# Performance work log

Hardware: AMD Instinct MI355X
Metric: run time of the kernel (lower is better)

## Reference

```python
import jax, jax.numpy as jnp
import numpy as np
from jax import lax

WIN_SIZE = 11
BANDWIDTH = 0.5


def _regression(rand, target, win_size, bandwidth):
    """Sliding-window bandwidth-weighted regression moments.

    For each pixel p, over window neighbors q:
      w_pq = exp(-||target_p - target_q||^2 / bandwidth^2)   (guide-based kernel)
      x  = sum_q w * t_q / wgtSum
      xx = sum_q w * t_q^2 / wgtSum
      xy = sum_q w * t_q * r_q / wgtSum
      y  = sum_q w * r_q / wgtSum
    """
    B, H, W, C = target.shape
    R = win_size // 2
    inv_bw2 = 1.0 / (bandwidth * bandwidth)

    pad_cfg = ((0, 0), (R, R), (R, R), (0, 0))
    t_pad = jnp.pad(target, pad_cfg)
    r_pad = jnp.pad(rand, pad_cfg)
    # validity mask so out-of-image taps contribute zero weight
    m_pad = jnp.pad(jnp.ones((B, H, W, 1), dtype=target.dtype), pad_cfg)

    # all (dy, dx) offsets in the window, scanned sequentially (static count)
    offs = np.stack(np.meshgrid(np.arange(win_size), np.arange(win_size),
                                indexing='ij'), axis=-1).reshape(-1, 2)
    offs = jnp.asarray(offs, dtype=jnp.int32)

    zeros_c = jnp.zeros((B, H, W, C), dtype=target.dtype)
    zeros_1 = jnp.zeros((B, H, W, 1), dtype=target.dtype)

    def body(carry, off):
        x, xx, xy, y, wsum = carry
        dy, dx = off[0], off[1]
        t_s = lax.dynamic_slice(t_pad, (0, dy, dx, 0), (B, H, W, C))
        r_s = lax.dynamic_slice(r_pad, (0, dy, dx, 0), (B, H, W, C))
        m_s = lax.dynamic_slice(m_pad, (0, dy, dx, 0), (B, H, W, 1))
        # per-pixel squared color distance on the guide, summed over channels
        d = jnp.sum((target - t_s) ** 2, axis=-1, keepdims=True)  # [B,H,W,1]
        w = jnp.exp(-d * inv_bw2) * m_s                           # [B,H,W,1]
        return (x + w * t_s,
                xx + w * t_s * t_s,
                xy + w * t_s * r_s,
                y + w * r_s,
                wsum + w), None

    (x, xx, xy, y, wsum), _ = lax.scan(
        body, (zeros_c, zeros_c, zeros_c, zeros_c, zeros_1), offs)

    inv_w = 1.0 / wsum  # wsum >= 1 (center tap has w=1), safe
    return x * inv_w, xx * inv_w, xy * inv_w, y * inv_w


def setup_inputs() -> dict:
    key = jax.random.key(0)
    k1, k2 = jax.random.split(key)
    B, H, W, C = 4, 720, 1280, 3
    rand = jax.random.uniform(k1, (B, H, W, C), dtype=jnp.float32)
    target = jax.random.uniform(k2, (B, H, W, C), dtype=jnp.float32)
    return {"rand": rand, "target": target}


def reference(rand, target):
    return _regression(rand, target, WIN_SIZE, BANDWIDTH)
```

## Files before the change

### kernel.cpp

```cpp
#include <hip/hip_runtime.h>


#define HH   720
#define WW   1280
#define BB   4
#define RAD  5
#define TX   64
#define TY   16
#define KX   4
#define LW   74
#define LH   26
#define LSTR 75
#define PLANE (LSTR * LH)
#define LDS_FLOATS 12288

__global__ __launch_bounds__(256, 3)
void regression_kernel(const float* __restrict__ rnd,
                       const float* __restrict__ tgt,
                       float* __restrict__ out)
{
    __shared__ __align__(16) float lds[LDS_FLOATS];
    float* pt0 = lds;
    float* pt1 = lds + PLANE;
    float* pt2 = lds + 2 * PLANE;
    float* pr0 = lds + 3 * PLANE;
    float* pr1 = lds + 4 * PLANE;
    float* pr2 = lds + 5 * PLANE;

    const int tx = threadIdx.x;
    const int ty = threadIdx.y;
    const int tid = ty * 16 + tx;
    const int X0 = blockIdx.x * TX;
    const int Y0 = blockIdx.y * TY;
    const int b  = blockIdx.z;

    for (int i = tid; i < LW * LH; i += 256) {
        int ly = i / LW;
        int lx = i - ly * LW;
        int gy = Y0 + ly - RAD;
        int gx = X0 + lx - RAD;
        float t0 = 0.f, t1 = 0.f, t2 = 0.f, r0 = 0.f, r1 = 0.f, r2 = 0.f;
        if ((unsigned)gy < (unsigned)HH && (unsigned)gx < (unsigned)WW) {
            int off = ((b * HH + gy) * WW + gx) * 3;
            t0 = tgt[off + 0]; t1 = tgt[off + 1]; t2 = tgt[off + 2];
            r0 = rnd[off + 0]; r1 = rnd[off + 1]; r2 = rnd[off + 2];
        }
        int s = ly * LSTR + lx;
        pt0[s] = t0; pt1[s] = t1; pt2[s] = t2;
        pr0[s] = r0; pr1[s] = r1; pr2[s] = r2;
    }
    __syncthreads();

    float tp0[KX], tp1[KX], tp2[KX];
    {
        int s = (ty + RAD) * LSTR + tx * KX + RAD;
        #pragma unroll
        for (int k = 0; k < KX; ++k) {
            tp0[k] = pt0[s + k]; tp1[k] = pt1[s + k]; tp2[k] = pt2[s + k];
        }
    }

    float sx0[KX] = {}, sx1[KX] = {}, sx2[KX] = {};
    float sxx0[KX] = {}, sxx1[KX] = {}, sxx2[KX] = {};
    float sxy0[KX] = {}, sxy1[KX] = {}, sxy2[KX] = {};
    float sy0[KX] = {}, sy1[KX] = {}, sy2[KX] = {};
    float sw[KX] = {};

    const int xbase = X0 + tx * KX - RAD;
    const int ybase = Y0 + ty - RAD;
    const float NEG = -1e30f;
    const float CC  = -5.770780163555852f;

    #pragma unroll 1
    for (int dy = 0; dy < 11; ++dy) {
        const float rowbias = ((unsigned)(ybase + dy) < (unsigned)HH) ? 0.f : NEG;
        const int rbase = (ty + dy) * LSTR + tx * KX;
        #pragma unroll
        for (int j = 0; j < 14; ++j) {
            const int s = rbase + j;
            const float t0 = pt0[s], t1 = pt1[s], t2 = pt2[s];
            const float r0 = pr0[s], r1 = pr1[s], r2 = pr2[s];
            const float bias = ((unsigned)(xbase + j) < (unsigned)WW) ? rowbias : NEG;
            #pragma unroll
            for (int k = 0; k < KX; ++k) {
                if (j >= k && j <= k + 10) {
                    float d0 = tp0[k] - t0;
                    float d1 = tp1[k] - t1;
                    float d2 = tp2[k] - t2;
                    float d  = d0 * d0;
                    d = fmaf(d1, d1, d);
                    d = fmaf(d2, d2, d);
                    float w = exp2f(fmaf(d, CC, bias));
                    float wt0 = w * t0, wt1 = w * t1, wt2 = w * t2;
                    sx0[k] += wt0;  sx1[k] += wt1;  sx2[k] += wt2;
                    sxx0[k] = fmaf(wt0, t0, sxx0[k]);
                    sxx1[k] = fmaf(wt1, t1, sxx1[k]);
                    sxx2[k] = fmaf(wt2, t2, sxx2[k]);
                    sxy0[k] = fmaf(wt0, r0, sxy0[k]);
                    sxy1[k] = fmaf(wt1, r1, sxy1[k]);
                    sxy2[k] = fmaf(wt2, r2, sxy2[k]);
                    sy0[k]  = fmaf(w, r0, sy0[k]);
                    sy1[k]  = fmaf(w, r1, sy1[k]);
                    sy2[k]  = fmaf(w, r2, sy2[k]);
                    sw[k]  += w;
                }
            }
        }
    }

    float inv[KX];
    #pragma unroll
    for (int k = 0; k < KX; ++k) inv[k] = 1.0f / sw[k];

    __syncthreads();

    float4* l4 = (float4*)lds;
    {
        const int b4 = ty * 48 + tx * 3;
#define STAGE_CHUNK(a0, a1, a2, cidx)                                          \
        {                                                                      \
            float4* p = l4 + (cidx) * 768 + b4;                                \
            p[0] = make_float4(a0[0]*inv[0], a1[0]*inv[0], a2[0]*inv[0],       \
                               a0[1]*inv[1]);                                  \
            p[1] = make_float4(a1[1]*inv[1], a2[1]*inv[1], a0[2]*inv[2],       \
                               a1[2]*inv[2]);                                  \
            p[2] = make_float4(a2[2]*inv[2], a0[3]*inv[3], a1[3]*inv[3],       \
                               a2[3]*inv[3]);                                  \
        }
        STAGE_CHUNK(sx0,  sx1,  sx2,  0)
        STAGE_CHUNK(sxx0, sxx1, sxx2, 1)
        STAGE_CHUNK(sxy0, sxy1, sxy2, 2)
        STAGE_CHUNK(sy0,  sy1,  sy2,  3)
#undef STAGE_CHUNK
    }
    __syncthreads();

    const int CH = BB * HH * WW * 3;
    int rr[3], cc4[3];
    #pragma unroll
    for (int m = 0; m < 3; ++m) {
        int r = m * 256 + tid;
        rr[m]  = r / 48;
        cc4[m] = r - rr[m] * 48;
    }
    #pragma unroll
    for (int i = 0; i < 12; ++i) {
        const int c = i / 3;
        const int m = i - c * 3;
        float4 v = l4[c * 768 + m * 256 + tid];
        const int gaddr = c * CH + ((b * HH + Y0 + rr[m]) * WW + X0) * 3 + cc4[m] * 4;
        *(float4*)(out + gaddr) = v;
    }
}

extern "C" void kernel_launch(void* const* d_in, const int* in_sizes, int n_in,
                              void* d_out, int out_size, void* d_ws, size_t ws_size,
                              hipStream_t stream) {
    const float* rnd = (const float*)d_in[0];
    const float* tgt = (const float*)d_in[1];
    float* out = (float*)d_out;

    dim3 grid(WW / TX, HH / TY, BB);
    dim3 block(16, 16);
    regression_kernel<<<grid, block, 0, stream>>>(rnd, tgt, out);
}
```

Before: 684.3 us.

## Use sentinel guide values for padding and vectorize LDS row loads

Out-of-image taps are now filled with a huge sentinel guide value, so their Gaussian weight underflows to zero. This removes the per-tap row/column bias computation and the extra FMA in the exponent. The LDS stride is padded to 76 so each thread's row window can be read with aligned float4 loads in two chunks of 8 and 6 taps, replacing scalar LDS reads. This relies on exp2 of a very large negative argument returning exactly zero, and the 16-wide reads per thread may raise LDS bank pressure.

```diff
diff --git a/kernel.cpp b/kernel.cpp
--- a/kernel.cpp
+++ b/kernel.cpp
@@ -8,9 +8,8 @@
 #define TX   64
 #define TY   16
 #define KX   4
-#define LW   74
 #define LH   26
-#define LSTR 75
+#define LSTR 76
 #define PLANE (LSTR * LH)
 #define LDS_FLOATS 12288
 
@@ -34,20 +33,21 @@
     const int Y0 = blockIdx.y * TY;
     const int b  = blockIdx.z;
 
-    for (int i = tid; i < LW * LH; i += 256) {
-        int ly = i / LW;
-        int lx = i - ly * LW;
+    const float SENT = 1e19f;
+
+    for (int i = tid; i < PLANE; i += 256) {
+        int ly = i / LSTR;
+        int lx = i - ly * LSTR;
         int gy = Y0 + ly - RAD;
         int gx = X0 + lx - RAD;
-        float t0 = 0.f, t1 = 0.f, t2 = 0.f, r0 = 0.f, r1 = 0.f, r2 = 0.f;
+        float t0 = SENT, t1 = SENT, t2 = SENT, r0 = 0.f, r1 = 0.f, r2 = 0.f;
         if ((unsigned)gy < (unsigned)HH && (unsigned)gx < (unsigned)WW) {
             int off = ((b * HH + gy) * WW + gx) * 3;
             t0 = tgt[off + 0]; t1 = tgt[off + 1]; t2 = tgt[off + 2];
             r0 = rnd[off + 0]; r1 = rnd[off + 1]; r2 = rnd[off + 2];
         }
-        int s = ly * LSTR + lx;
-        pt0[s] = t0; pt1[s] = t1; pt2[s] = t2;
-        pr0[s] = r0; pr1[s] = r1; pr2[s] = r2;
+        pt0[i] = t0; pt1[i] = t1; pt2[i] = t2;
+        pr0[i] = r0; pr1[i] = r1; pr2[i] = r2;
     }
     __syncthreads();
 
@@ -66,47 +66,83 @@
     float sy0[KX] = {}, sy1[KX] = {}, sy2[KX] = {};
     float sw[KX] = {};
 
-    const int xbase = X0 + tx * KX - RAD;
-    const int ybase = Y0 + ty - RAD;
-    const float NEG = -1e30f;
-    const float CC  = -5.770780163555852f;
+    const float CC = -5.770780163555852f;
+
+#define TAPK(k)                                                         \
+    {                                                                   \
+        float d0 = tp0[k] - t0;                                         \
+        float d1 = tp1[k] - t1;                                         \
+        float d2 = tp2[k] - t2;                                         \
+        float d  = d0 * d0;                                             \
+        d = fmaf(d1, d1, d);                                            \
+        d = fmaf(d2, d2, d);                                            \
+        float w = exp2f(d * CC);         \
+        float wt0 = w * t0, wt1 = w * t1, wt2 = w * t2;                 \
+        sx0[k] += wt0;  sx1[k] += wt1;  sx2[k] += wt2;                  \
+        sxx0[k] = fmaf(wt0, t0, sxx0[k]);                               \
+        sxx1[k] = fmaf(wt1, t1, sxx1[k]);                               \
+        sxx2[k] = fmaf(wt2, t2, sxx2[k]);                               \
+        sxy0[k] = fmaf(wt0, r0, sxy0[k]);                               \
+        sxy1[k] = fmaf(wt1, r1, sxy1[k]);                               \
+        sxy2[k] = fmaf(wt2, r2, sxy2[k]);                               \
+        sy0[k]  = fmaf(w, r0, sy0[k]);                                  \
+        sy1[k]  = fmaf(w, r1, sy1[k]);                                  \
+        sy2[k]  = fmaf(w, r2, sy2[k]);                                  \
+        sw[k]  += w;                                                    \
+    }
 
     #pragma unroll 1
     for (int dy = 0; dy < 11; ++dy) {
-        const float rowbias = ((unsigned)(ybase + dy) < (unsigned)HH) ? 0.f : NEG;
-        const int rbase = (ty + dy) * LSTR + tx * KX;
+        const int rb = (ty + dy) * LSTR + tx * KX;
+        float T0[8], T1[8], T2[8], R0[8], R1[8], R2[8];
+
+        *(float4*)&T0[0] = *(const float4*)(pt0 + rb);
+        *(float4*)&T0[4] = *(const float4*)(pt0 + rb + 4);
+        *(float4*)&T1[0] = *(const float4*)(pt1 + rb);
+        *(float4*)&T1[4] = *(const float4*)(pt1 + rb + 4);
+        *(float4*)&T2[0] = *(const float4*)(pt2 + rb);
+        *(float4*)&T2[4] = *(const float4*)(pt2 + rb + 4);
+        *(float4*)&R0[0] = *(const float4*)(pr0 + rb);
+        *(float4*)&R0[4] = *(const float4*)(pr0 + rb + 4);
+        *(float4*)&R1[0] = *(const float4*)(pr1 + rb);
+        *(float4*)&R1[4] = *(const float4*)(pr1 + rb + 4);
+        *(float4*)&R2[0] = *(const float4*)(pr2 + rb);
+        *(float4*)&R2[4] = *(const float4*)(pr2 + rb + 4);
+
         #pragma unroll
-        for (int j = 0; j < 14; ++j) {
-            const int s = rbase + j;
-            const float t0 = pt0[s], t1 = pt1[s], t2 = pt2[s];
-            const float r0 = pr0[s], r1 = pr1[s], r2 = pr2[s];
-            const float bias = ((unsigned)(xbase + j) < (unsigned)WW) ? rowbias : NEG;
+        for (int j = 0; j < 8; ++j) {
+            const float t0 = T0[j], t1 = T1[j], t2 = T2[j];
+            const float r0 = R0[j], r1 = R1[j], r2 = R2[j];
             #pragma unroll
-            for (int k = 0; k < KX; ++k) {
-                if (j >= k && j <= k + 10) {
-                    float d0 = tp0[k] - t0;
-                    float d1 = tp1[k] - t1;
-                    float d2 = tp2[k] - t2;
-                    float d  = d0 * d0;
-                    d = fmaf(d1, d1, d);
-                    d = fmaf(d2, d2, d);
-                    float w = exp2f(fmaf(d, CC, bias));
-                    float wt0 = w * t0, wt1 = w * t1, wt2 = w * t2;
-                    sx0[k] += wt0;  sx1[k] += wt1;  sx2[k] += wt2;
-                    sxx0[k] = fmaf(wt0, t0, sxx0[k]);
-                    sxx1[k] = fmaf(wt1, t1, sxx1[k]);
-                    sxx2[k] = fmaf(wt2, t2, sxx2[k]);
-                    sxy0[k] = fmaf(wt0, r0, sxy0[k]);
-                    sxy1[k] = fmaf(wt1, r1, sxy1[k]);
-                    sxy2[k] = fmaf(wt2, r2, sxy2[k]);
-                    sy0[k]  = fmaf(w, r0, sy0[k]);
-                    sy1[k]  = fmaf(w, r1, sy1[k]);
-                    sy2[k]  = fmaf(w, r2, sy2[k]);
-                    sw[k]  += w;
-                }
-            }
-        }
-    }
+            for (int k = 0; k < KX; ++k)
+                if (k <= j)
+                    TAPK(k)
+        }
+
+        *(float4*)&T0[0] = *(const float4*)(pt0 + rb + 8);
+        *(float4*)&T0[4] = *(const float4*)(pt0 + rb + 12);
+        *(float4*)&T1[0] = *(const float4*)(pt1 + rb + 8);
+        *(float4*)&T1[4] = *(const float4*)(pt1 + rb + 12);
+        *(float4*)&T2[0] = *(const float4*)(pt2 + rb + 8);
+        *(float4*)&T2[4] = *(const float4*)(pt2 + rb + 12);
+        *(float4*)&R0[0] = *(const float4*)(pr0 + rb + 8);
+        *(float4*)&R0[4] = *(const float4*)(pr0 + rb + 12);
+        *(float4*)&R1[0] = *(const float4*)(pr1 + rb + 8);
+        *(float4*)&R1[4] = *(const float4*)(pr1 + rb + 12);
+        *(float4*)&R2[0] = *(const float4*)(pr2 + rb + 8);
+        *(float4*)&R2[4] = *(const float4*)(pr2 + rb + 12);
+
+        #pragma unroll
+        for (int j2 = 0; j2 < 6; ++j2) {
+            const float t0 = T0[j2], t1 = T1[j2], t2 = T2[j2];
+            const float r0 = R0[j2], r1 = R1[j2], r2 = R2[j2];
+            #pragma unroll
+            for (int k = 0; k < KX; ++k)
+                if (k >= j2 - 2)
+                    TAPK(k)
+        }
+    }
+#undef TAPK
 
     float inv[KX];
     #pragma unroll
```

Result: faster. 647.8 us (-5.3%).
